# Kernel tuning notes

Hardware: AMD Instinct MI355X
Metric: run time of the kernel (lower is better)

The kernel has to match this reference:

```python
import jax, jax.numpy as jnp
import numpy as np

B = 32768

def _lin(x, w, b):
    return x @ w.T + b

def setup_inputs() -> dict:
    key = jax.random.key(0)
    ks = iter(jax.random.split(key, 40))
    def rn(shape, s=0.05):
        return jax.random.normal(next(ks), shape, dtype=jnp.float32) * s
    inp = {
        'img_feat': jax.random.normal(next(ks), (B, 256), dtype=jnp.float32),
        'instruction_idx': jax.random.randint(next(ks), (B, 1), 0, 4),
        '_hx': jax.random.normal(next(ks), (B, 256), dtype=jnp.float32),
        '_cx': jax.random.normal(next(ks), (B, 256), dtype=jnp.float32),
        'query': jax.random.normal(next(ks), (B, 256), dtype=jnp.float32),
        # parameters
        'emb': rn((4, 25), 1.0),
        'w_ta': rn((256, 25)), 'b_ta': rn((256,)),
        'w_ih': rn((1024, 512)), 'w_hh': rn((1024, 256)),
        'b_ih': rn((1024,)), 'b_hh': rn((1024,)),
        'w_q': rn((256, 256)), 'b_q': rn((256,)),
        'w_k': rn((256, 256)), 'b_k': rn((256,)),
        'w_ba': rn((512, 512)), 'b_ba': rn((512,)),
        'w_at': rn((256, 512)), 'b_at': rn((256,)),
        'w_p1': rn((128, 256)), 'b_p1': rn((128,)),
        'w_p2': rn((64, 128)), 'b_p2': rn((64,)),
        'w_p': rn((3, 64)), 'b_p': rn((3,)),
        'w_v1': rn((64, 256)), 'b_v1': rn((64,)),
        'w_v2': rn((32, 64)), 'b_v2': rn((32,)),
        'w_v': rn((1, 32)), 'b_v': rn((1,)),
    }
    return inp

def reference(img_feat, instruction_idx, _hx, _cx, query,
              emb, w_ta, b_ta, w_ih, w_hh, b_ih, b_hh,
              w_q, b_q, w_k, b_k, w_ba, b_ba, w_at, b_at,
              w_p1, b_p1, w_p2, b_p2, w_p, b_p,
              w_v1, b_v1, w_v2, b_v2, w_v, b_v):
    # embedding lookup [B,1,25] -> [B,25]
    we = emb[instruction_idx].reshape(instruction_idx.shape[0], -1)
    gated_att = jax.nn.sigmoid(_lin(we, w_ta, b_ta))          # [B,256]
    gated_fusion = img_feat * gated_att                        # [B,256]
    lstm_input = jnp.concatenate([gated_fusion, gated_att], 1) # [B,512]
    # LSTMCell (PyTorch gate order: i, f, g, o)
    gates = lstm_input @ w_ih.T + b_ih + _hx @ w_hh.T + b_hh   # [B,1024]
    i, f, g, o = jnp.split(gates, 4, axis=1)
    cx = jax.nn.sigmoid(f) * _cx + jax.nn.sigmoid(i) * jnp.tanh(g)
    hx = jax.nn.sigmoid(o) * jnp.tanh(cx)
    mlp_input = jnp.concatenate([gated_fusion, hx], 1)         # [B,512]
    mlp_attn = jax.nn.relu(_lin(mlp_input, w_ba, b_ba))        # [B,512]
    key_, val = jnp.split(mlp_attn, 2, axis=1)                 # [B,256] each
    w_q_out = jax.nn.relu(_lin(query, w_q, b_q))
    w_k_out = jax.nn.relu(_lin(key_, w_k, b_k))
    u_t = jnp.tanh(w_q_out + w_k_out)
    attention_vector = u_t * val
    attn_weight = jnp.concatenate([attention_vector, hx], 1)   # [B,512]
    attn_weight = jax.nn.relu(_lin(attn_weight, w_at, b_at))   # [B,256]
    pol = jax.nn.relu(_lin(attn_weight, w_p1, b_p1))
    pol = jax.nn.relu(_lin(pol, w_p2, b_p2))
    valh = jax.nn.relu(_lin(attn_weight, w_v1, b_v1))
    valh = jax.nn.relu(_lin(valh, w_v2, b_v2))
    return (_lin(valh, w_v, b_v), _lin(pol, w_p, b_p), hx, cx)
```

## Files before the change

kernel.cpp:

```cpp
#include <hip/hip_runtime.h>

typedef unsigned short u16;
typedef __bf16 bf16x8 __attribute__((ext_vector_type(8)));
typedef float f32x4 __attribute__((ext_vector_type(4)));
typedef u16 u16x8 __attribute__((ext_vector_type(8)));
typedef u16 u16x4 __attribute__((ext_vector_type(4)));

#define TM 64
#define LDP 264
#define BTOT 32768

#define OFF_WIH 0
#define OFF_WHH 524288
#define OFF_WQ  786432
#define OFF_WK  851968
#define OFF_WBA 917504
#define OFF_WAT 1179648
#define OFF_WP1 1310720
#define OFF_WP2 1343488
#define OFF_WV1 1351680
#define OFF_WV2 1368064

__device__ __forceinline__ float b2f(u16 h) {
    union { unsigned int u; float f; } v; v.u = ((unsigned int)h) << 16; return v.f;
}
__device__ __forceinline__ u16 f2b(float f) {
    union { float f; unsigned int u; } v; v.f = f;
    unsigned int u = v.u + 0x7fffu + ((v.u >> 16) & 1u);
    return (u16)(u >> 16);
}
__device__ __forceinline__ float sigm(float x) { return 1.0f / (1.0f + __expf(-x)); }
__device__ __forceinline__ float tanhfast(float x) { return 1.0f - 2.0f / (__expf(2.0f * x) + 1.0f); }
__device__ __forceinline__ float relu(float x) { return x > 0.0f ? x : 0.0f; }
__device__ __forceinline__ bf16x8 ld8(const u16* p) { return *(const bf16x8*)p; }
__device__ __forceinline__ f32x4 mfma16(bf16x8 a, bf16x8 b, f32x4 c) {
    return __builtin_amdgcn_mfma_f32_16x16x32_bf16(a, b, c, 0, 0, 0);
}

__device__ __forceinline__ bool detect_f32(const void* imgp) {
    const unsigned int* w = (const unsigned int*)imgp;
    int hits = 0;
    #pragma unroll
    for (int i = 0; i < 16; ++i) {
        int e0 = (w[i] >> 7) & 0xFF;
        hits += (e0 >= 100 && e0 <= 140) ? 1 : 0;
    }
    return hits < 10;
}

__device__ __forceinline__ float ldin(const void* p, size_t i, bool f32) {
    return f32 ? ((const float*)p)[i] : b2f(((const u16*)p)[i]);
}
__device__ __forceinline__ void stout_nt(void* o, size_t i, float v, bool f32) {
    if (f32) __builtin_nontemporal_store(v, (float*)o + i);
    else ((u16*)o)[i] = f2b(v);
}
__device__ __forceinline__ f32x4 ld4(const void* p, size_t i, bool f32) {
    if (f32) return __builtin_nontemporal_load((const f32x4*)((const float*)p + i));
    u16x4 q = *(const u16x4*)((const u16*)p + i);
    f32x4 r;
    #pragma unroll
    for (int j = 0; j < 4; ++j) r[j] = b2f(q[j]);
    return r;
}
__device__ __forceinline__ void st4(void* o, size_t i, f32x4 v, bool f32) {
    if (f32) __builtin_nontemporal_store(v, (f32x4*)((float*)o + i));
    else {
        u16x4 p;
        #pragma unroll
        for (int j = 0; j < 4; ++j) p[j] = f2b(v[j]);
        *(u16x4*)((u16*)o + i) = p;
    }
}
__device__ __forceinline__ bf16x8 ldg8f_nt(const void* p, size_t i, bool f32) {
    u16 t[8];
    if (f32) {
        const f32x4* q = (const f32x4*)((const float*)p + i);
        f32x4 a = __builtin_nontemporal_load(q);
        f32x4 b = __builtin_nontemporal_load(q + 1);
        #pragma unroll
        for (int j = 0; j < 4; ++j) { t[j] = f2b(a[j]); t[4 + j] = f2b(b[j]); }
    } else {
        *(u16x8*)t = *(const u16x8*)((const u16*)p + i);
    }
    return *(bf16x8*)t;
}

struct CvtArgs {
    const void* src[10];
    unsigned int nchunk[10];
    unsigned int off8[10];
    unsigned int Kdim[10];
    const void* det;
};

__global__ __launch_bounds__(256) void cvt_weights(CvtArgs a, u16* ws) {
    const bool f32 = detect_f32(a.det);
    const int p = blockIdx.x;
    const void* s = a.src[p];
    const unsigned int K = a.Kdim[p];
    const unsigned int KK = K >> 5;
    const unsigned int msk = KK - 1u;
    const unsigned int sh = 31 - __clz((int)KK);
    const unsigned int n = a.nchunk[p];
    for (unsigned int g = blockIdx.y * blockDim.x + threadIdx.x; g < n;
         g += gridDim.y * blockDim.x) {
        const unsigned int lane = g & 63u;
        const unsigned int fi = g >> 6;
        const unsigned int kk = fi & msk;
        const unsigned int tn = fi >> sh;
        const unsigned int row = tn * 16u + (lane & 15u);
        const unsigned int col = kk * 32u + ((lane >> 4) << 3);
        const size_t si = (size_t)row * K + col;
        u16 t[8];
        if (f32) {
            const f32x4* q = (const f32x4*)((const float*)s + si);
            f32x4 va = __builtin_nontemporal_load(q);
            f32x4 vb = __builtin_nontemporal_load(q + 1);
            #pragma unroll
            for (int j = 0; j < 4; ++j) { t[j] = f2b(va[j]); t[4 + j] = f2b(vb[j]); }
        } else {
            *(u16x8*)t = *(const u16x8*)((const u16*)s + si);
        }
        ((u16x8*)ws)[a.off8[p] + g] = *(u16x8*)t;
    }
}

__global__ __launch_bounds__(1024, 2) void ac_fused(
    const void* __restrict__ img, const int* __restrict__ insn,
    const void* __restrict__ hx_in, const void* __restrict__ cx_in,
    const void* __restrict__ query,
    const void* __restrict__ emb, const void* __restrict__ w_ta, const void* __restrict__ b_ta,
    const void* __restrict__ b_ih, const void* __restrict__ b_hh,
    const void* __restrict__ b_q, const void* __restrict__ b_k,
    const void* __restrict__ b_ba, const void* __restrict__ b_at,
    const void* __restrict__ b_p1, const void* __restrict__ b_p2,
    const void* __restrict__ w_p3, const void* __restrict__ b_p3,
    const void* __restrict__ b_v1, const void* __restrict__ b_v2,
    const void* __restrict__ w_v3, const void* __restrict__ b_v3,
    const u16* __restrict__ wsb, void* __restrict__ out)
{
    __shared__ __align__(16) u16 sGF[TM * LDP];
    __shared__ __align__(16) u16 sHX0[TM * LDP];
    __shared__ __align__(16) u16 sHX1[TM * LDP];
    __shared__ __align__(16) u16 sKEY[TM * LDP];
    __shared__ __align__(16) u16 sG[4 * LDP];
    __shared__ int sIDX[TM];

    const bool isf32 = detect_f32(img);
    const int tid  = threadIdx.x;
    const int lane = tid & 63;
    const int wv   = tid >> 6;
    const int l15  = lane & 15;
    const int quad = lane >> 4;
    const int q8   = quad * 8;
    const int q4   = quad * 4;
    const int ln8  = lane * 8;
    const int row0 = blockIdx.x * TM;

    if (tid < TM) sIDX[tid] = insn[row0 + tid];
    {
        int e = tid >> 8, n = tid & 255;
        float acc = ldin(b_ta, n, isf32);
        #pragma unroll
        for (int k = 0; k < 25; ++k)
            acc += ldin(emb, e * 25 + k, isf32) * ldin(w_ta, n * 25 + k, isf32);
        sG[e * LDP + n] = f2b(sigm(acc));
    }
    __syncthreads();

    for (int it = tid; it < TM * 32; it += 1024) {
        int r = it >> 5, c0 = (it & 31) << 3;
        int e = sIDX[r];
        u16x8 gv = *(const u16x8*)(sG + e * LDP + c0);
        float iv[8], hv[8];
        const size_t base = (size_t)(row0 + r) * 256 + c0;
        if (isf32) {
            const f32x4* ip = (const f32x4*)((const float*)img + base);
            const f32x4* hp = (const f32x4*)((const float*)hx_in + base);
            f32x4 a0 = __builtin_nontemporal_load(ip);
            f32x4 a1 = __builtin_nontemporal_load(ip + 1);
            f32x4 b0 = __builtin_nontemporal_load(hp);
            f32x4 b1 = __builtin_nontemporal_load(hp + 1);
            #pragma unroll
            for (int j = 0; j < 4; ++j) {
                iv[j] = a0[j]; iv[4 + j] = a1[j];
                hv[j] = b0[j]; hv[4 + j] = b1[j];
            }
        } else {
            u16x8 i8 = *(const u16x8*)((const u16*)img + base);
            u16x8 h8 = *(const u16x8*)((const u16*)hx_in + base);
            #pragma unroll
            for (int j = 0; j < 8; ++j) { iv[j] = b2f(i8[j]); hv[j] = b2f(h8[j]); }
        }
        u16x8 ov, hvv;
        #pragma unroll
        for (int j = 0; j < 8; ++j) {
            ov[j] = f2b(iv[j] * b2f(gv[j]));
            hvv[j] = f2b(hv[j]);
        }
        *(u16x8*)(sGF + r * LDP + c0) = ov;
        *(u16x8*)(sHX0 + r * LDP + c0) = hvv;
    }
    __syncthreads();

    {
        int eIdx[4];
        #pragma unroll
        for (int m = 0; m < 4; ++m) eIdx[m] = sIDX[m * 16 + l15];
        const u16* bih0 = wsb + OFF_WIH + ln8;
        const u16* bhh0 = wsb + OFF_WHH + ln8;
        const int c = wv;
        f32x4 acc[4][4] = {};
        #pragma unroll
        for (int kk = 0; kk < 8; ++kk) {
            bf16x8 a[4], b[4];
            #pragma unroll
            for (int m = 0; m < 4; ++m) a[m] = ld8(sGF + (m * 16 + l15) * LDP + kk * 32 + q8);
            #pragma unroll
            for (int g = 0; g < 4; ++g) b[g] = ld8(bih0 + (size_t)((g * 16 + c) * 16 + kk) * 512);
            #pragma unroll
            for (int g = 0; g < 4; ++g)
                #pragma unroll
                for (int m = 0; m < 4; ++m) acc[g][m] = mfma16(b[g], a[m], acc[g][m]);
        }
        #pragma unroll
        for (int kk = 0; kk < 8; ++kk) {
            bf16x8 a[4], b[4];
            #pragma unroll
            for (int m = 0; m < 4; ++m) a[m] = ld8(sG + eIdx[m] * LDP + kk * 32 + q8);
            #pragma unroll
            for (int g = 0; g < 4; ++g) b[g] = ld8(bih0 + (size_t)((g * 16 + c) * 16 + 8 + kk) * 512);
            #pragma unroll
            for (int g = 0; g < 4; ++g)
                #pragma unroll
                for (int m = 0; m < 4; ++m) acc[g][m] = mfma16(b[g], a[m], acc[g][m]);
        }
        #pragma unroll
        for (int kk = 0; kk < 8; ++kk) {
            bf16x8 a[4], b[4];
            #pragma unroll
            for (int m = 0; m < 4; ++m) a[m] = ld8(sHX0 + (m * 16 + l15) * LDP + kk * 32 + q8);
            #pragma unroll
            for (int g = 0; g < 4; ++g) b[g] = ld8(bhh0 + (size_t)((g * 16 + c) * 8 + kk) * 512);
            #pragma unroll
            for (int g = 0; g < 4; ++g)
                #pragma unroll
                for (int m = 0; m < 4; ++m) acc[g][m] = mfma16(b[g], a[m], acc[g][m]);
        }
        const int nbase = c * 16 + q4;
        float bI[4], bF[4], bG[4], bO[4];
        #pragma unroll
        for (int r = 0; r < 4; ++r) {
            bI[r] = ldin(b_ih,       nbase + r, isf32) + ldin(b_hh,       nbase + r, isf32);
            bF[r] = ldin(b_ih, 256 + nbase + r, isf32) + ldin(b_hh, 256 + nbase + r, isf32);
            bG[r] = ldin(b_ih, 512 + nbase + r, isf32) + ldin(b_hh, 512 + nbase + r, isf32);
            bO[r] = ldin(b_ih, 768 + nbase + r, isf32) + ldin(b_hh, 768 + nbase + r, isf32);
        }
        #pragma unroll
        for (int m = 0; m < 4; ++m) {
            const int batch = m * 16 + l15;
            const size_t gbase = (size_t)(row0 + batch) * 256 + nbase;
            f32x4 cxo = ld4(cx_in, gbase, isf32);
            f32x4 hnv, cnv; u16x4 hpk;
            #pragma unroll
            for (int r = 0; r < 4; ++r) {
                const float iv = sigm(acc[0][m][r] + bI[r]);
                const float fv = sigm(acc[1][m][r] + bF[r]);
                const float gv = tanhfast(acc[2][m][r] + bG[r]);
                const float ov = sigm(acc[3][m][r] + bO[r]);
                const float cn = fv * cxo[r] + iv * gv;
                const float hn = ov * tanhfast(cn);
                cnv[r] = cn; hnv[r] = hn; hpk[r] = f2b(hn);
            }
            st4(out, (size_t)(4 * BTOT) + gbase, hnv, isf32);
            st4(out, (size_t)(4 * BTOT) + (size_t)256 * BTOT + gbase, cnv, isf32);
            *(u16x4*)(sHX1 + batch * LDP + nbase) = hpk;
        }
    }
    __syncthreads();

    {
        f32x4 acc[2][4] = {};
        const u16* bb0 = wsb + OFF_WBA + ln8;
        #pragma unroll
        for (int kk = 0; kk < 8; ++kk) {
            bf16x8 a[4], b[2];
            #pragma unroll
            for (int m = 0; m < 4; ++m) a[m] = ld8(sGF + (m * 16 + l15) * LDP + kk * 32 + q8);
            #pragma unroll
            for (int t = 0; t < 2; ++t) b[t] = ld8(bb0 + (size_t)((wv * 2 + t) * 16 + kk) * 512);
            #pragma unroll
            for (int t = 0; t < 2; ++t)
                #pragma unroll
                for (int m = 0; m < 4; ++m) acc[t][m] = mfma16(b[t], a[m], acc[t][m]);
        }
        #pragma unroll
        for (int kk = 0; kk < 8; ++kk) {
            bf16x8 a[4], b[2];
            #pragma unroll
            for (int m = 0; m < 4; ++m) a[m] = ld8(sHX1 + (m * 16 + l15) * LDP + kk * 32 + q8);
            #pragma unroll
            for (int t = 0; t < 2; ++t) b[t] = ld8(bb0 + (size_t)((wv * 2 + t) * 16 + 8 + kk) * 512);
            #pragma unroll
            for (int t = 0; t < 2; ++t)
                #pragma unroll
                for (int m = 0; m < 4; ++m) acc[t][m] = mfma16(b[t], a[m], acc[t][m]);
        }
        #pragma unroll
        for (int t = 0; t < 2; ++t) {
            const int colb = (wv * 2 + t) * 16 + q4;
            float bb[4];
            #pragma unroll
            for (int r = 0; r < 4; ++r) bb[r] = ldin(b_ba, colb + r, isf32);
            u16* dst = (colb < 256) ? (sKEY + colb) : (sHX0 + (colb - 256));
            #pragma unroll
            for (int m = 0; m < 4; ++m) {
                u16x4 pk;
                #pragma unroll
                for (int r = 0; r < 4; ++r) pk[r] = f2b(relu(acc[t][m][r] + bb[r]));
                *(u16x4*)(dst + (m * 16 + l15) * LDP) = pk;
            }
        }
    }
    __syncthreads();

    {
        f32x4 cq[4] = {}, ck[4] = {};
        const u16* bq0 = wsb + OFF_WQ + ln8;
        const u16* bk0 = wsb + OFF_WK + ln8;
        #pragma unroll
        for (int kk = 0; kk < 8; ++kk) {
            bf16x8 aq[4], ak[4], bqf, bkf;
            #pragma unroll
            for (int m = 0; m < 4; ++m) {
                aq[m] = ldg8f_nt(query, (size_t)(row0 + m * 16 + l15) * 256 + kk * 32 + q8, isf32);
                ak[m] = ld8(sKEY + (m * 16 + l15) * LDP + kk * 32 + q8);
            }
            bqf = ld8(bq0 + (size_t)(wv * 8 + kk) * 512);
            bkf = ld8(bk0 + (size_t)(wv * 8 + kk) * 512);
            #pragma unroll
            for (int m = 0; m < 4; ++m) {
                cq[m] = mfma16(bqf, aq[m], cq[m]);
                ck[m] = mfma16(bkf, ak[m], ck[m]);
            }
        }
        const int nbase = wv * 16 + q4;
        float bqv[4], bkv[4];
        #pragma unroll
        for (int r = 0; r < 4; ++r) {
            bqv[r] = ldin(b_q, nbase + r, isf32);
            bkv[r] = ldin(b_k, nbase + r, isf32);
        }
        #pragma unroll
        for (int m = 0; m < 4; ++m) {
            const int batch = m * 16 + l15;
            u16x4 vv = *(const u16x4*)(sHX0 + batch * LDP + nbase);
            u16x4 pk;
            #pragma unroll
            for (int r = 0; r < 4; ++r) {
                const float u = tanhfast(relu(cq[m][r] + bqv[r]) + relu(ck[m][r] + bkv[r]));
                pk[r] = f2b(u * b2f(vv[r]));
            }
            *(u16x4*)(sGF + batch * LDP + nbase) = pk;
        }
    }
    __syncthreads();

    {
        f32x4 acc[4] = {};
        const u16* bb0 = wsb + OFF_WAT + ln8;
        #pragma unroll
        for (int kk = 0; kk < 8; ++kk) {
            bf16x8 a[4], b;
            #pragma unroll
            for (int m = 0; m < 4; ++m) a[m] = ld8(sGF + (m * 16 + l15) * LDP + kk * 32 + q8);
            b = ld8(bb0 + (size_t)(wv * 16 + kk) * 512);
            #pragma unroll
            for (int m = 0; m < 4; ++m) acc[m] = mfma16(b, a[m], acc[m]);
        }
        #pragma unroll
        for (int kk = 0; kk < 8; ++kk) {
            bf16x8 a[4], b;
            #pragma unroll
            for (int m = 0; m < 4; ++m) a[m] = ld8(sHX1 + (m * 16 + l15) * LDP + kk * 32 + q8);
            b = ld8(bb0 + (size_t)(wv * 16 + 8 + kk) * 512);
            #pragma unroll
            for (int m = 0; m < 4; ++m) acc[m] = mfma16(b, a[m], acc[m]);
        }
        const int nbase = wv * 16 + q4;
        float bb[4];
        #pragma unroll
        for (int r = 0; r < 4; ++r) bb[r] = ldin(b_at, nbase + r, isf32);
        #pragma unroll
        for (int m = 0; m < 4; ++m) {
            u16x4 pk;
            #pragma unroll
            for (int r = 0; r < 4; ++r) pk[r] = f2b(relu(acc[m][r] + bb[r]));
            *(u16x4*)(sKEY + (m * 16 + l15) * LDP + nbase) = pk;
        }
    }
    __syncthreads();

    {
        const int m = wv & 3, half = wv >> 2;
        const int batch = m * 16 + l15;
        bf16x8 afr[8];
        #pragma unroll
        for (int kk = 0; kk < 8; ++kk) afr[kk] = ld8(sKEY + batch * LDP + kk * 32 + q8);
        {
            f32x4 acc[2] = {};
            #pragma unroll
            for (int kk = 0; kk < 8; ++kk)
                #pragma unroll
                for (int t = 0; t < 2; ++t)
                    acc[t] = mfma16(ld8(wsb + OFF_WP1 + (size_t)((half * 2 + t) * 8 + kk) * 512 + ln8), afr[kk], acc[t]);
            #pragma unroll
            for (int t = 0; t < 2; ++t) {
                const int colb = (half * 2 + t) * 16 + q4;
                u16x4 pk;
                #pragma unroll
                for (int r = 0; r < 4; ++r) pk[r] = f2b(relu(acc[t][r] + ldin(b_p1, colb + r, isf32)));
                *(u16x4*)(sHX0 + batch * LDP + colb) = pk;
            }
        }
        {
            f32x4 acc = {};
            #pragma unroll
            for (int kk = 0; kk < 8; ++kk)
                acc = mfma16(ld8(wsb + OFF_WV1 + (size_t)(half * 8 + kk) * 512 + ln8), afr[kk], acc);
            const int colb = half * 16 + q4;
            u16x4 pk;
            #pragma unroll
            for (int r = 0; r < 4; ++r) pk[r] = f2b(relu(acc[r] + ldin(b_v1, colb + r, isf32)));
            *(u16x4*)(sHX0 + batch * LDP + 128 + colb) = pk;
        }
    }
    __syncthreads();

    {
        const int m = wv & 3, half = wv >> 2;
        const int batch = m * 16 + l15;
        const u16* a0 = sHX0 + batch * LDP;
        bf16x8 ap[4], av2[2];
        #pragma unroll
        for (int kk = 0; kk < 4; ++kk) ap[kk] = ld8(a0 + kk * 32 + q8);
        #pragma unroll
        for (int kk = 0; kk < 2; ++kk) av2[kk] = ld8(a0 + 128 + kk * 32 + q8);
        {
            f32x4 acc = {};
            #pragma unroll
            for (int kk = 0; kk < 4; ++kk)
                acc = mfma16(ld8(wsb + OFF_WP2 + (size_t)(half * 4 + kk) * 512 + ln8), ap[kk], acc);
            const int colb = half * 16 + q4;
            u16x4 pk;
            #pragma unroll
            for (int r = 0; r < 4; ++r) pk[r] = f2b(relu(acc[r] + ldin(b_p2, colb + r, isf32)));
            *(u16x4*)(sGF + batch * LDP + colb) = pk;
        }
        if (half < 2) {
            f32x4 acc = {};
            #pragma unroll
            for (int kk = 0; kk < 2; ++kk)
                acc = mfma16(ld8(wsb + OFF_WV2 + (size_t)(half * 2 + kk) * 512 + ln8), av2[kk], acc);
            const int colb = half * 16 + q4;
            u16x4 pk;
            #pragma unroll
            for (int r = 0; r < 4; ++r) pk[r] = f2b(relu(acc[r] + ldin(b_v2, colb + r, isf32)));
            *(u16x4*)(sGF + batch * LDP + 64 + colb) = pk;
        }
    }
    __syncthreads();

    if (tid < TM * 4) {
        const int r = tid >> 2, o = tid & 3;
        const int grow = row0 + r;
        const u16* rowp = sGF + r * LDP;
        if (o < 3) {
            float acc = ldin(b_p3, o, isf32);
            #pragma unroll
            for (int k = 0; k < 64; ++k) acc += b2f(rowp[k]) * ldin(w_p3, o * 64 + k, isf32);
            stout_nt(out, (size_t)BTOT + (size_t)grow * 3 + o, acc, isf32);
        } else {
            float acc = ldin(b_v3, 0, isf32);
            #pragma unroll
            for (int k = 0; k < 32; ++k) acc += b2f(rowp[64 + k]) * ldin(w_v3, k, isf32);
            stout_nt(out, (size_t)grow, acc, isf32);
        }
    }
}

extern "C" void kernel_launch(void* const* d_in, const int* in_sizes, int n_in,
                              void* d_out, int out_size, void* d_ws, size_t ws_size,
                              hipStream_t stream) {
    u16* ws = (u16*)d_ws;

    CvtArgs ca;
    const int srcIdx[10] = {8, 9, 12, 14, 16, 18, 20, 22, 26, 28};
    const unsigned int ns[10]   = {524288, 262144, 65536, 65536, 262144, 131072, 32768, 8192, 16384, 2048};
    const unsigned int off[10]  = {OFF_WIH, OFF_WHH, OFF_WQ, OFF_WK, OFF_WBA, OFF_WAT, OFF_WP1, OFF_WP2, OFF_WV1, OFF_WV2};
    const unsigned int kd[10]   = {512, 256, 256, 256, 512, 512, 256, 128, 256, 64};
    for (int i = 0; i < 10; ++i) {
        ca.src[i] = d_in[srcIdx[i]];
        ca.nchunk[i] = ns[i] / 8;
        ca.off8[i] = off[i] / 8;
        ca.Kdim[i] = kd[i];
    }
    ca.det = d_in[0];
    cvt_weights<<<dim3(10, 64), dim3(256), 0, stream>>>(ca, ws);

    ac_fused<<<dim3(BTOT / TM), dim3(1024), 0, stream>>>(
        d_in[0], (const int*)d_in[1], d_in[2], d_in[3], d_in[4],
        d_in[5], d_in[6], d_in[7],
        d_in[10], d_in[11],
        d_in[13], d_in[15],
        d_in[17], d_in[19],
        d_in[21], d_in[23],
        d_in[24], d_in[25],
        d_in[27], d_in[29],
        d_in[30], d_in[31],
        (const u16*)d_ws, d_out);
}
```

Measured before the change: 421.9 us.

## Double-buffer operand loads in fused GEMM stages and overlap query prefetch with barrier

Each MFMA stage now uses explicit ping-pong register buffers, so the next k-step's LDS and weight loads are issued before the current step's MFMAs. The separate k-sections of each GEMM are merged into one software-pipelined loop. The first query/weight fragments for the Q/K stage are prefetched before the barrier. The weight conversion kernel now iterates over source-contiguous elements for coalesced reads and scatters into the tiled layout. Extra live registers may raise pressure at the kernel's 1024-thread, 2-block launch bounds and risk spills.

```diff
diff --git a/kernel.cpp b/kernel.cpp
--- a/kernel.cpp
+++ b/kernel.cpp
@@ -99,19 +99,17 @@
     const int p = blockIdx.x;
     const void* s = a.src[p];
     const unsigned int K = a.Kdim[p];
-    const unsigned int KK = K >> 5;
-    const unsigned int msk = KK - 1u;
-    const unsigned int sh = 31 - __clz((int)KK);
+    const unsigned int sh = 31 - __clz((int)(K >> 5));
+    const unsigned int cpr = K >> 3;
+    const unsigned int csh = sh + 2;
     const unsigned int n = a.nchunk[p];
-    for (unsigned int g = blockIdx.y * blockDim.x + threadIdx.x; g < n;
-         g += gridDim.y * blockDim.x) {
-        const unsigned int lane = g & 63u;
-        const unsigned int fi = g >> 6;
-        const unsigned int kk = fi & msk;
-        const unsigned int tn = fi >> sh;
-        const unsigned int row = tn * 16u + (lane & 15u);
-        const unsigned int col = kk * 32u + ((lane >> 4) << 3);
-        const size_t si = (size_t)row * K + col;
+    for (unsigned int e = blockIdx.y * blockDim.x + threadIdx.x; e < n;
+         e += gridDim.y * blockDim.x) {
+        const unsigned int row  = e >> csh;
+        const unsigned int colc = e & (cpr - 1u);
+        const unsigned int g = ((((row >> 4) << sh) + (colc >> 2)) << 6)
+                             + ((colc & 3u) << 4) + (row & 15u);
+        const size_t si = ((size_t)row << (csh + 3)) + (colc << 3);
         u16 t[8];
         if (f32) {
             const f32x4* q = (const f32x4*)((const float*)s + si);
@@ -211,43 +209,48 @@
         const u16* bih0 = wsb + OFF_WIH + ln8;
         const u16* bhh0 = wsb + OFF_WHH + ln8;
         const int c = wv;
+
+        auto t1LA = [&](int s, bf16x8 (&a)[4]) {
+            const int sec = s >> 3, kq = (s & 7) * 32 + q8;
+            #pragma unroll
+            for (int m = 0; m < 4; ++m) {
+                const u16* src = (sec == 0) ? (sGF + (m * 16 + l15) * LDP + kq)
+                               : (sec == 1) ? (sG + eIdx[m] * LDP + kq)
+                                            : (sHX0 + (m * 16 + l15) * LDP + kq);
+                a[m] = ld8(src);
+            }
+        };
+        auto t1LB = [&](int s, bf16x8 (&b)[4]) {
+            const int sec = s >> 3, kk = s & 7;
+            #pragma unroll
+            for (int g = 0; g < 4; ++g)
+                b[g] = (sec < 2)
+                     ? ld8(bih0 + (size_t)((g * 16 + c) * 16 + sec * 8 + kk) * 512)
+                     : ld8(bhh0 + (size_t)((g * 16 + c) * 8 + kk) * 512);
+        };
+
         f32x4 acc[4][4] = {};
-        #pragma unroll
-        for (int kk = 0; kk < 8; ++kk) {
-            bf16x8 a[4], b[4];
-            #pragma unroll
-            for (int m = 0; m < 4; ++m) a[m] = ld8(sGF + (m * 16 + l15) * LDP + kk * 32 + q8);
-            #pragma unroll
-            for (int g = 0; g < 4; ++g) b[g] = ld8(bih0 + (size_t)((g * 16 + c) * 16 + kk) * 512);
-            #pragma unroll
-            for (int g = 0; g < 4; ++g)
-                #pragma unroll
-                for (int m = 0; m < 4; ++m) acc[g][m] = mfma16(b[g], a[m], acc[g][m]);
-        }
-        #pragma unroll
-        for (int kk = 0; kk < 8; ++kk) {
-            bf16x8 a[4], b[4];
-            #pragma unroll
-            for (int m = 0; m < 4; ++m) a[m] = ld8(sG + eIdx[m] * LDP + kk * 32 + q8);
-            #pragma unroll
-            for (int g = 0; g < 4; ++g) b[g] = ld8(bih0 + (size_t)((g * 16 + c) * 16 + 8 + kk) * 512);
-            #pragma unroll
-            for (int g = 0; g < 4; ++g)
-                #pragma unroll
-                for (int m = 0; m < 4; ++m) acc[g][m] = mfma16(b[g], a[m], acc[g][m]);
-        }
-        #pragma unroll
-        for (int kk = 0; kk < 8; ++kk) {
-            bf16x8 a[4], b[4];
-            #pragma unroll
-            for (int m = 0; m < 4; ++m) a[m] = ld8(sHX0 + (m * 16 + l15) * LDP + kk * 32 + q8);
-            #pragma unroll
-            for (int g = 0; g < 4; ++g) b[g] = ld8(bhh0 + (size_t)((g * 16 + c) * 8 + kk) * 512);
-            #pragma unroll
-            for (int g = 0; g < 4; ++g)
-                #pragma unroll
-                for (int m = 0; m < 4; ++m) acc[g][m] = mfma16(b[g], a[m], acc[g][m]);
-        }
+        bf16x8 aP[4], bP[4], aN[4], bN[4];
+        t1LA(0, aP); t1LB(0, bP);
+        #pragma unroll
+        for (int s = 0; s < 24; ++s) {
+            if (s + 1 < 24) {
+                if (s & 1) { t1LA(s + 1, aP); t1LB(s + 1, bP); }
+                else       { t1LA(s + 1, aN); t1LB(s + 1, bN); }
+            }
+            if (s & 1) {
+                #pragma unroll
+                for (int g = 0; g < 4; ++g)
+                    #pragma unroll
+                    for (int m = 0; m < 4; ++m) acc[g][m] = mfma16(bN[g], aN[m], acc[g][m]);
+            } else {
+                #pragma unroll
+                for (int g = 0; g < 4; ++g)
+                    #pragma unroll
+                    for (int m = 0; m < 4; ++m) acc[g][m] = mfma16(bP[g], aP[m], acc[g][m]);
+            }
+        }
+
         const int nbase = c * 16 + q4;
         float bI[4], bF[4], bG[4], bO[4];
         #pragma unroll
@@ -281,31 +284,42 @@
     __syncthreads();
 
     {
+        const u16* bb0 = wsb + OFF_WBA + ln8;
+        auto t2LA = [&](int s, bf16x8 (&a)[4]) {
+            const int sec = s >> 3, kq = (s & 7) * 32 + q8;
+            const u16* base = (sec == 0) ? sGF : sHX1;
+            #pragma unroll
+            for (int m = 0; m < 4; ++m) a[m] = ld8(base + (m * 16 + l15) * LDP + kq);
+        };
+        auto t2LB = [&](int s, bf16x8 (&b)[2]) {
+            const int sec = s >> 3, kk = s & 7;
+            #pragma unroll
+            for (int t = 0; t < 2; ++t)
+                b[t] = ld8(bb0 + (size_t)((wv * 2 + t) * 16 + sec * 8 + kk) * 512);
+        };
+
         f32x4 acc[2][4] = {};
-        const u16* bb0 = wsb + OFF_WBA + ln8;
-        #pragma unroll
-        for (int kk = 0; kk < 8; ++kk) {
-            bf16x8 a[4], b[2];
-            #pragma unroll
-            for (int m = 0; m < 4; ++m) a[m] = ld8(sGF + (m * 16 + l15) * LDP + kk * 32 + q8);
-            #pragma unroll
-            for (int t = 0; t < 2; ++t) b[t] = ld8(bb0 + (size_t)((wv * 2 + t) * 16 + kk) * 512);
-            #pragma unroll
-            for (int t = 0; t < 2; ++t)
-                #pragma unroll
-                for (int m = 0; m < 4; ++m) acc[t][m] = mfma16(b[t], a[m], acc[t][m]);
-        }
-        #pragma unroll
-        for (int kk = 0; kk < 8; ++kk) {
-            bf16x8 a[4], b[2];
-            #pragma unroll
-            for (int m = 0; m < 4; ++m) a[m] = ld8(sHX1 + (m * 16 + l15) * LDP + kk * 32 + q8);
-            #pragma unroll
-            for (int t = 0; t < 2; ++t) b[t] = ld8(bb0 + (size_t)((wv * 2 + t) * 16 + 8 + kk) * 512);
-            #pragma unroll
-            for (int t = 0; t < 2; ++t)
-                #pragma unroll
-                for (int m = 0; m < 4; ++m) acc[t][m] = mfma16(b[t], a[m], acc[t][m]);
+        {
+            bf16x8 aP[4], aN[4], bP[2], bN[2];
+            t2LA(0, aP); t2LB(0, bP);
+            #pragma unroll
+            for (int s = 0; s < 16; ++s) {
+                if (s + 1 < 16) {
+                    if (s & 1) { t2LA(s + 1, aP); t2LB(s + 1, bP); }
+                    else       { t2LA(s + 1, aN); t2LB(s + 1, bN); }
+                }
+                if (s & 1) {
+                    #pragma unroll
+                    for (int t = 0; t < 2; ++t)
+                        #pragma unroll
+                        for (int m = 0; m < 4; ++m) acc[t][m] = mfma16(bN[t], aN[m], acc[t][m]);
+                } else {
+                    #pragma unroll
+                    for (int t = 0; t < 2; ++t)
+                        #pragma unroll
+                        for (int m = 0; m < 4; ++m) acc[t][m] = mfma16(bP[t], aP[m], acc[t][m]);
+                }
+            }
         }
         #pragma unroll
         for (int t = 0; t < 2; ++t) {
@@ -322,27 +336,57 @@
                 *(u16x4*)(dst + (m * 16 + l15) * LDP) = pk;
             }
         }
-    }
-    __syncthreads();
-
-    {
-        f32x4 cq[4] = {}, ck[4] = {};
+
         const u16* bq0 = wsb + OFF_WQ + ln8;
         const u16* bk0 = wsb + OFF_WK + ln8;
-        #pragma unroll
-        for (int kk = 0; kk < 8; ++kk) {
-            bf16x8 aq[4], ak[4], bqf, bkf;
-            #pragma unroll
-            for (int m = 0; m < 4; ++m) {
-                aq[m] = ldg8f_nt(query, (size_t)(row0 + m * 16 + l15) * 256 + kk * 32 + q8, isf32);
-                ak[m] = ld8(sKEY + (m * 16 + l15) * LDP + kk * 32 + q8);
-            }
-            bqf = ld8(bq0 + (size_t)(wv * 8 + kk) * 512);
-            bkf = ld8(bk0 + (size_t)(wv * 8 + kk) * 512);
-            #pragma unroll
-            for (int m = 0; m < 4; ++m) {
-                cq[m] = mfma16(bqf, aq[m], cq[m]);
-                ck[m] = mfma16(bkf, ak[m], ck[m]);
+        bf16x8 aqP[4], aqN[4];
+        bf16x8 bqP, bkP, bqN, bkN;
+        #pragma unroll
+        for (int m = 0; m < 4; ++m)
+            aqP[m] = ldg8f_nt(query, (size_t)(row0 + m * 16 + l15) * 256 + q8, isf32);
+        bqP = ld8(bq0 + (size_t)(wv * 8) * 512);
+        bkP = ld8(bk0 + (size_t)(wv * 8) * 512);
+
+        __syncthreads();
+
+        f32x4 cq[4] = {}, ck[4] = {};
+        bf16x8 akP[4], akN[4];
+        #pragma unroll
+        for (int m = 0; m < 4; ++m) akP[m] = ld8(sKEY + (m * 16 + l15) * LDP + q8);
+        #pragma unroll
+        for (int s = 0; s < 8; ++s) {
+            if (s + 1 < 8) {
+                const int kq = (s + 1) * 32 + q8;
+                if (s & 1) {
+                    #pragma unroll
+                    for (int m = 0; m < 4; ++m) {
+                        aqP[m] = ldg8f_nt(query, (size_t)(row0 + m * 16 + l15) * 256 + kq, isf32);
+                        akP[m] = ld8(sKEY + (m * 16 + l15) * LDP + kq);
+                    }
+                    bqP = ld8(bq0 + (size_t)(wv * 8 + s + 1) * 512);
+                    bkP = ld8(bk0 + (size_t)(wv * 8 + s + 1) * 512);
+                } else {
+                    #pragma unroll
+                    for (int m = 0; m < 4; ++m) {
+                        aqN[m] = ldg8f_nt(query, (size_t)(row0 + m * 16 + l15) * 256 + kq, isf32);
+                        akN[m] = ld8(sKEY + (m * 16 + l15) * LDP + kq);
+                    }
+                    bqN = ld8(bq0 + (size_t)(wv * 8 + s + 1) * 512);
+                    bkN = ld8(bk0 + (size_t)(wv * 8 + s + 1) * 512);
+                }
+            }
+            if (s & 1) {
+                #pragma unroll
+                for (int m = 0; m < 4; ++m) {
+                    cq[m] = mfma16(bqN, aqN[m], cq[m]);
+                    ck[m] = mfma16(bkN, akN[m], ck[m]);
+                }
+            } else {
+                #pragma unroll
+                for (int m = 0; m < 4; ++m) {
+                    cq[m] = mfma16(bqP, aqP[m], cq[m]);
+                    ck[m] = mfma16(bkP, akP[m], ck[m]);
+                }
             }
         }
         const int nbase = wv * 16 + q4;
@@ -368,25 +412,36 @@
     __syncthreads();
 
     {
+        const u16* bb0 = wsb + OFF_WAT + ln8;
+        auto t4LA = [&](int s, bf16x8 (&a)[4]) {
+            const int sec = s >> 3, kq = (s & 7) * 32 + q8;
+            const u16* base = (sec == 0) ? sGF : sHX1;
+            #pragma unroll
+            for (int m = 0; m < 4; ++m) a[m] = ld8(base + (m * 16 + l15) * LDP + kq);
+        };
         f32x4 acc[4] = {};
-        const u16* bb0 = wsb + OFF_WAT + ln8;
-        #pragma unroll
-        for (int kk = 0; kk < 8; ++kk) {
-            bf16x8 a[4], b;
-            #pragma unroll
-            for (int m = 0; m < 4; ++m) a[m] = ld8(sGF + (m * 16 + l15) * LDP + kk * 32 + q8);
-            b = ld8(bb0 + (size_t)(wv * 16 + kk) * 512);
-            #pragma unroll
-            for (int m = 0; m < 4; ++m) acc[m] = mfma16(b, a[m], acc[m]);
-        }
-        #pragma unroll
-        for (int kk = 0; kk < 8; ++kk) {
-            bf16x8 a[4], b;
-            #pragma unroll
-            for (int m = 0; m < 4; ++m) a[m] = ld8(sHX1 + (m * 16 + l15) * LDP + kk * 32 + q8);
-            b = ld8(bb0 + (size_t)(wv * 16 + 8 + kk) * 512);
-            #pragma unroll
-            for (int m = 0; m < 4; ++m) acc[m] = mfma16(b, a[m], acc[m]);
+        bf16x8 aP[4], aN[4], bP, bN;
+        t4LA(0, aP);
+        bP = ld8(bb0 + (size_t)(wv * 16) * 512);
+        #pragma unroll
+        for (int s = 0; s < 16; ++s) {
+            if (s + 1 < 16) {
+                const int sec = (s + 1) >> 3, kk = (s + 1) & 7;
+                if (s & 1) {
+                    t4LA(s + 1, aP);
+                    bP = ld8(bb0 + (size_t)(wv * 16 + sec * 8 + kk) * 512);
+                } else {
+                    t4LA(s + 1, aN);
+                    bN = ld8(bb0 + (size_t)(wv * 16 + sec * 8 + kk) * 512);
+                }
+            }
+            if (s & 1) {
+                #pragma unroll
+                for (int m = 0; m < 4; ++m) acc[m] = mfma16(bN, aN[m], acc[m]);
+            } else {
+                #pragma unroll
+                for (int m = 0; m < 4; ++m) acc[m] = mfma16(bP, aP[m], acc[m]);
+            }
         }
         const int nbase = wv * 16 + q4;
         float bb[4];
```

New measurement: 452.5 us. 7.2% more time.

## Prefetch next-stage weights and inputs before barriers and defer LSTM output stores

Applied to the files above, without the earlier changes.

Before each __syncthreads, every stage now issues the first global loads of the next stage's weight and activation fragments (W_ba, W_q/W_k plus the query tile, W_at, W_p1/W_v1, W_p2/W_v2), so their latency overlaps the barrier wait. The cx load is moved ahead of the LSTM gate GEMM, and the hx/cx global stores are held in registers and written after the barrier, overlapping with the next GEMM. The tiny final-head weights are staged once into shared memory instead of being re-read from global in the inner loop. In exchange, register pressure rises, which may cut occupancy or cause spills.

```diff
diff --git a/kernel.cpp b/kernel.cpp
--- a/kernel.cpp
+++ b/kernel.cpp
@@ -145,6 +145,7 @@
     __shared__ __align__(16) u16 sHX1[TM * LDP];
     __shared__ __align__(16) u16 sKEY[TM * LDP];
     __shared__ __align__(16) u16 sG[4 * LDP];
+    __shared__ float sW3[224];
     __shared__ int sIDX[TM];
 
     const bool isf32 = detect_f32(img);
@@ -204,6 +205,7 @@
     }
     __syncthreads();
 
+    f32x4 hnS[4], cnS[4];
     {
         int eIdx[4];
         #pragma unroll
@@ -211,6 +213,12 @@
         const u16* bih0 = wsb + OFF_WIH + ln8;
         const u16* bhh0 = wsb + OFF_WHH + ln8;
         const int c = wv;
+        const int nbase = c * 16 + q4;
+        f32x4 cxo[4];
+        #pragma unroll
+        for (int m = 0; m < 4; ++m)
+            cxo[m] = ld4(cx_in, (size_t)(row0 + m * 16 + l15) * 256 + nbase, isf32);
+
         f32x4 acc[4][4] = {};
         #pragma unroll
         for (int kk = 0; kk < 8; ++kk) {
@@ -248,7 +256,6 @@
                 #pragma unroll
                 for (int m = 0; m < 4; ++m) acc[g][m] = mfma16(b[g], a[m], acc[g][m]);
         }
-        const int nbase = c * 16 + q4;
         float bI[4], bF[4], bG[4], bO[4];
         #pragma unroll
         for (int r = 0; r < 4; ++r) {
@@ -260,48 +267,63 @@
         #pragma unroll
         for (int m = 0; m < 4; ++m) {
             const int batch = m * 16 + l15;
-            const size_t gbase = (size_t)(row0 + batch) * 256 + nbase;
-            f32x4 cxo = ld4(cx_in, gbase, isf32);
-            f32x4 hnv, cnv; u16x4 hpk;
+            u16x4 hpk;
             #pragma unroll
             for (int r = 0; r < 4; ++r) {
                 const float iv = sigm(acc[0][m][r] + bI[r]);
                 const float fv = sigm(acc[1][m][r] + bF[r]);
                 const float gv = tanhfast(acc[2][m][r] + bG[r]);
                 const float ov = sigm(acc[3][m][r] + bO[r]);
-                const float cn = fv * cxo[r] + iv * gv;
+                const float cn = fv * cxo[m][r] + iv * gv;
                 const float hn = ov * tanhfast(cn);
-                cnv[r] = cn; hnv[r] = hn; hpk[r] = f2b(hn);
-            }
-            st4(out, (size_t)(4 * BTOT) + gbase, hnv, isf32);
-            st4(out, (size_t)(4 * BTOT) + (size_t)256 * BTOT + gbase, cnv, isf32);
+                cnS[m][r] = cn; hnS[m][r] = hn; hpk[r] = f2b(hn);
+            }
             *(u16x4*)(sHX1 + batch * LDP + nbase) = hpk;
         }
     }
-    __syncthreads();
-
-    {
+
+    const u16* bba0 = wsb + OFF_WBA + ln8;
+    bf16x8 h2a[4], h2b[2];
+    #pragma unroll
+    for (int m = 0; m < 4; ++m) h2a[m] = ld8(sGF + (m * 16 + l15) * LDP + q8);
+    #pragma unroll
+    for (int t = 0; t < 2; ++t) h2b[t] = ld8(bba0 + (size_t)((wv * 2 + t) * 16) * 512);
+    __syncthreads();
+
+    {
+        {
+            const int nbase = wv * 16 + q4;
+            #pragma unroll
+            for (int m = 0; m < 4; ++m) {
+                const size_t gbase = (size_t)(row0 + m * 16 + l15) * 256 + nbase;
+                st4(out, (size_t)(4 * BTOT) + gbase, hnS[m], isf32);
+                st4(out, (size_t)(4 * BTOT) + (size_t)256 * BTOT + gbase, cnS[m], isf32);
+            }
+        }
         f32x4 acc[2][4] = {};
-        const u16* bb0 = wsb + OFF_WBA + ln8;
+        #pragma unroll
+        for (int t = 0; t < 2; ++t)
+            #pragma unroll
+            for (int m = 0; m < 4; ++m) acc[t][m] = mfma16(h2b[t], h2a[m], acc[t][m]);
+        #pragma unroll
+        for (int kk = 1; kk < 8; ++kk) {
+            bf16x8 a[4], b[2];
+            #pragma unroll
+            for (int m = 0; m < 4; ++m) a[m] = ld8(sGF + (m * 16 + l15) * LDP + kk * 32 + q8);
+            #pragma unroll
+            for (int t = 0; t < 2; ++t) b[t] = ld8(bba0 + (size_t)((wv * 2 + t) * 16 + kk) * 512);
+            #pragma unroll
+            for (int t = 0; t < 2; ++t)
+                #pragma unroll
+                for (int m = 0; m < 4; ++m) acc[t][m] = mfma16(b[t], a[m], acc[t][m]);
+        }
         #pragma unroll
         for (int kk = 0; kk < 8; ++kk) {
             bf16x8 a[4], b[2];
             #pragma unroll
-            for (int m = 0; m < 4; ++m) a[m] = ld8(sGF + (m * 16 + l15) * LDP + kk * 32 + q8);
-            #pragma unroll
-            for (int t = 0; t < 2; ++t) b[t] = ld8(bb0 + (size_t)((wv * 2 + t) * 16 + kk) * 512);
-            #pragma unroll
-            for (int t = 0; t < 2; ++t)
-                #pragma unroll
-                for (int m = 0; m < 4; ++m) acc[t][m] = mfma16(b[t], a[m], acc[t][m]);
-        }
-        #pragma unroll
-        for (int kk = 0; kk < 8; ++kk) {
-            bf16x8 a[4], b[2];
-            #pragma unroll
             for (int m = 0; m < 4; ++m) a[m] = ld8(sHX1 + (m * 16 + l15) * LDP + kk * 32 + q8);
             #pragma unroll
-            for (int t = 0; t < 2; ++t) b[t] = ld8(bb0 + (size_t)((wv * 2 + t) * 16 + 8 + kk) * 512);
+            for (int t = 0; t < 2; ++t) b[t] = ld8(bba0 + (size_t)((wv * 2 + t) * 16 + 8 + kk) * 512);
             #pragma unroll
             for (int t = 0; t < 2; ++t)
                 #pragma unroll
@@ -323,14 +345,31 @@
             }
         }
     }
+
+    const u16* bq0 = wsb + OFF_WQ + ln8;
+    const u16* bk0 = wsb + OFF_WK + ln8;
+    bf16x8 h3aq[4], h3bq, h3bk;
+    #pragma unroll
+    for (int m = 0; m < 4; ++m)
+        h3aq[m] = ldg8f_nt(query, (size_t)(row0 + m * 16 + l15) * 256 + q8, isf32);
+    h3bq = ld8(bq0 + (size_t)(wv * 8) * 512);
+    h3bk = ld8(bk0 + (size_t)(wv * 8) * 512);
     __syncthreads();
 
     {
         f32x4 cq[4] = {}, ck[4] = {};
-        const u16* bq0 = wsb + OFF_WQ + ln8;
-        const u16* bk0 = wsb + OFF_WK + ln8;
-        #pragma unroll
-        for (int kk = 0; kk < 8; ++kk) {
+        {
+            bf16x8 ak0[4];
+            #pragma unroll
+            for (int m = 0; m < 4; ++m) ak0[m] = ld8(sKEY + (m * 16 + l15) * LDP + q8);
+            #pragma unroll
+            for (int m = 0; m < 4; ++m) {
+                cq[m] = mfma16(h3bq, h3aq[m], cq[m]);
+                ck[m] = mfma16(h3bk, ak0[m], ck[m]);
+            }
+        }
+        #pragma unroll
+        for (int kk = 1; kk < 8; ++kk) {
             bf16x8 aq[4], ak[4], bqf, bkf;
             #pragma unroll
             for (int m = 0; m < 4; ++m) {
@@ -365,26 +404,38 @@
             *(u16x4*)(sGF + batch * LDP + nbase) = pk;
         }
     }
+
+    const u16* bat0 = wsb + OFF_WAT + ln8;
+    bf16x8 h4b0 = ld8(bat0 + (size_t)(wv * 16) * 512);
+    bf16x8 h4b1 = ld8(bat0 + (size_t)(wv * 16 + 1) * 512);
     __syncthreads();
 
     {
         f32x4 acc[4] = {};
-        const u16* bb0 = wsb + OFF_WAT + ln8;
+        #pragma unroll
+        for (int kk = 0; kk < 2; ++kk) {
+            bf16x8 a[4];
+            #pragma unroll
+            for (int m = 0; m < 4; ++m) a[m] = ld8(sGF + (m * 16 + l15) * LDP + kk * 32 + q8);
+            const bf16x8 b = (kk == 0) ? h4b0 : h4b1;
+            #pragma unroll
+            for (int m = 0; m < 4; ++m) acc[m] = mfma16(b, a[m], acc[m]);
+        }
+        #pragma unroll
+        for (int kk = 2; kk < 8; ++kk) {
+            bf16x8 a[4], b;
+            #pragma unroll
+            for (int m = 0; m < 4; ++m) a[m] = ld8(sGF + (m * 16 + l15) * LDP + kk * 32 + q8);
+            b = ld8(bat0 + (size_t)(wv * 16 + kk) * 512);
+            #pragma unroll
+            for (int m = 0; m < 4; ++m) acc[m] = mfma16(b, a[m], acc[m]);
+        }
         #pragma unroll
         for (int kk = 0; kk < 8; ++kk) {
             bf16x8 a[4], b;
             #pragma unroll
-            for (int m = 0; m < 4; ++m) a[m] = ld8(sGF + (m * 16 + l15) * LDP + kk * 32 + q8);
-            b = ld8(bb0 + (size_t)(wv * 16 + kk) * 512);
-            #pragma unroll
-            for (int m = 0; m < 4; ++m) acc[m] = mfma16(b, a[m], acc[m]);
-        }
-        #pragma unroll
-        for (int kk = 0; kk < 8; ++kk) {
-            bf16x8 a[4], b;
-            #pragma unroll
             for (int m = 0; m < 4; ++m) a[m] = ld8(sHX1 + (m * 16 + l15) * LDP + kk * 32 + q8);
-            b = ld8(bb0 + (size_t)(wv * 16 + 8 + kk) * 512);
+            b = ld8(bat0 + (size_t)(wv * 16 + 8 + kk) * 512);
             #pragma unroll
             for (int m = 0; m < 4; ++m) acc[m] = mfma16(b, a[m], acc[m]);
         }
@@ -400,24 +451,34 @@
             *(u16x4*)(sKEY + (m * 16 + l15) * LDP + nbase) = pk;
         }
     }
-    __syncthreads();
-
-    {
-        const int m = wv & 3, half = wv >> 2;
-        const int batch = m * 16 + l15;
+
+    const int t56m = wv & 3, t56h = wv >> 2;
+    bf16x8 h5p0 = ld8(wsb + OFF_WP1 + (size_t)((t56h * 2 + 0) * 8) * 512 + ln8);
+    bf16x8 h5p1 = ld8(wsb + OFF_WP1 + (size_t)((t56h * 2 + 1) * 8) * 512 + ln8);
+    bf16x8 h5v0 = ld8(wsb + OFF_WV1 + (size_t)(t56h * 8) * 512 + ln8);
+    __syncthreads();
+
+    bf16x8 h6p[4], h6v[2];
+    {
+        if (tid < 224)
+            sW3[tid] = (tid < 192) ? ldin(w_p3, tid, isf32)
+                                   : ldin(w_v3, tid - 192, isf32);
+        const int batch = t56m * 16 + l15;
         bf16x8 afr[8];
         #pragma unroll
         for (int kk = 0; kk < 8; ++kk) afr[kk] = ld8(sKEY + batch * LDP + kk * 32 + q8);
         {
             f32x4 acc[2] = {};
-            #pragma unroll
-            for (int kk = 0; kk < 8; ++kk)
+            acc[0] = mfma16(h5p0, afr[0], acc[0]);
+            acc[1] = mfma16(h5p1, afr[0], acc[1]);
+            #pragma unroll
+            for (int kk = 1; kk < 8; ++kk)
                 #pragma unroll
                 for (int t = 0; t < 2; ++t)
-                    acc[t] = mfma16(ld8(wsb + OFF_WP1 + (size_t)((half * 2 + t) * 8 + kk) * 512 + ln8), afr[kk], acc[t]);
+                    acc[t] = mfma16(ld8(wsb + OFF_WP1 + (size_t)((t56h * 2 + t) * 8 + kk) * 512 + ln8), afr[kk], acc[t]);
             #pragma unroll
             for (int t = 0; t < 2; ++t) {
-                const int colb = (half * 2 + t) * 16 + q4;
+                const int colb = (t56h * 2 + t) * 16 + q4;
                 u16x4 pk;
                 #pragma unroll
                 for (int r = 0; r < 4; ++r) pk[r] = f2b(relu(acc[t][r] + ldin(b_p1, colb + r, isf32)));
@@ -426,21 +487,27 @@
         }
         {
             f32x4 acc = {};
-            #pragma unroll
-            for (int kk = 0; kk < 8; ++kk)
-                acc = mfma16(ld8(wsb + OFF_WV1 + (size_t)(half * 8 + kk) * 512 + ln8), afr[kk], acc);
-            const int colb = half * 16 + q4;
+            acc = mfma16(h5v0, afr[0], acc);
+            #pragma unroll
+            for (int kk = 1; kk < 8; ++kk)
+                acc = mfma16(ld8(wsb + OFF_WV1 + (size_t)(t56h * 8 + kk) * 512 + ln8), afr[kk], acc);
+            const int colb = t56h * 16 + q4;
             u16x4 pk;
             #pragma unroll
             for (int r = 0; r < 4; ++r) pk[r] = f2b(relu(acc[r] + ldin(b_v1, colb + r, isf32)));
             *(u16x4*)(sHX0 + batch * LDP + 128 + colb) = pk;
         }
-    }
-    __syncthreads();
-
-    {
-        const int m = wv & 3, half = wv >> 2;
-        const int batch = m * 16 + l15;
+        #pragma unroll
+        for (int kk = 0; kk < 4; ++kk)
+            h6p[kk] = ld8(wsb + OFF_WP2 + (size_t)(t56h * 4 + kk) * 512 + ln8);
+        #pragma unroll
+        for (int kk = 0; kk < 2; ++kk)
+            h6v[kk] = ld8(wsb + OFF_WV2 + (size_t)(t56h * 2 + kk) * 512 + ln8);
+    }
+    __syncthreads();
+
+    {
+        const int batch = t56m * 16 + l15;
         const u16* a0 = sHX0 + batch * LDP;
         bf16x8 ap[4], av2[2];
         #pragma unroll
@@ -450,20 +517,18 @@
         {
             f32x4 acc = {};
             #pragma unroll
-            for (int kk = 0; kk < 4; ++kk)
-                acc = mfma16(ld8(wsb + OFF_WP2 + (size_t)(half * 4 + kk) * 512 + ln8), ap[kk], acc);
-            const int colb = half * 16 + q4;
+            for (int kk = 0; kk < 4; ++kk) acc = mfma16(h6p[kk], ap[kk], acc);
+            const int colb = t56h * 16 + q4;
             u16x4 pk;
             #pragma unroll
             for (int r = 0; r < 4; ++r) pk[r] = f2b(relu(acc[r] + ldin(b_p2, colb + r, isf32)));
             *(u16x4*)(sGF + batch * LDP + colb) = pk;
         }
-        if (half < 2) {
+        if (t56h < 2) {
             f32x4 acc = {};
             #pragma unroll
-            for (int kk = 0; kk < 2; ++kk)
-                acc = mfma16(ld8(wsb + OFF_WV2 + (size_t)(half * 2 + kk) * 512 + ln8), av2[kk], acc);
-            const int colb = half * 16 + q4;
+            for (int kk = 0; kk < 2; ++kk) acc = mfma16(h6v[kk], av2[kk], acc);
+            const int colb = t56h * 16 + q4;
             u16x4 pk;
             #pragma unroll
             for (int r = 0; r < 4; ++r) pk[r] = f2b(relu(acc[r] + ldin(b_v2, colb + r, isf32)));
@@ -479,12 +544,12 @@
         if (o < 3) {
             float acc = ldin(b_p3, o, isf32);
             #pragma unroll
-            for (int k = 0; k < 64; ++k) acc += b2f(rowp[k]) * ldin(w_p3, o * 64 + k, isf32);
+            for (int k = 0; k < 64; ++k) acc += b2f(rowp[k]) * sW3[o * 64 + k];
             stout_nt(out, (size_t)BTOT + (size_t)grow * 3 + o, acc, isf32);
         } else {
             float acc = ldin(b_v3, 0, isf32);
             #pragma unroll
-            for (int k = 0; k < 32; ++k) acc += b2f(rowp[64 + k]) * ldin(w_v3, k, isf32);
+            for (int k = 0; k < 32; ++k) acc += b2f(rowp[64 + k]) * sW3[192 + k];
             stout_nt(out, (size_t)grow, acc, isf32);
         }
     }
```

Result: slower. 439.8 us (+4.2%).

## Precompute gate table in prep kernel, coalesce weight conversion, prefetch inputs early

Applied to the files above, without the earlier changes.

The 4x256 sigmoid gate table, which every block of the fused kernel used to recompute, is now built once by an extra block in the weight-conversion kernel and stored in the workspace, so fused blocks only copy it. The weight conversion loop now walks the source row-major for coalesced reads and scatters writes into the MFMA tile layout. The fused kernel also issues its img/hx loads before the first barrier, so their latency overlaps the index and table setup. In exchange the loads are held in more registers across the barrier, and the writes in the conversion kernel are scattered.

```diff
diff --git a/kernel.cpp b/kernel.cpp
--- a/kernel.cpp
+++ b/kernel.cpp
@@ -20,6 +20,7 @@
 #define OFF_WP2 1343488
 #define OFF_WV1 1351680
 #define OFF_WV2 1368064
+#define OFF_G   1370112
 
 __device__ __forceinline__ float b2f(u16 h) {
     union { unsigned int u; float f; } v; v.u = ((unsigned int)h) << 16; return v.f;
@@ -91,32 +92,46 @@
     unsigned int nchunk[10];
     unsigned int off8[10];
     unsigned int Kdim[10];
+    const void* emb;
+    const void* w_ta;
+    const void* b_ta;
     const void* det;
 };
 
 __global__ __launch_bounds__(256) void cvt_weights(CvtArgs a, u16* ws) {
     const bool f32 = detect_f32(a.det);
     const int p = blockIdx.x;
+    if (p == 10) {
+        if (blockIdx.y == 0) {
+            for (int j = threadIdx.x; j < 1024; j += 256) {
+                int e = j >> 8, n = j & 255;
+                float acc = ldin(a.b_ta, n, f32);
+                #pragma unroll
+                for (int k = 0; k < 25; ++k)
+                    acc += ldin(a.emb, e * 25 + k, f32) * ldin(a.w_ta, n * 25 + k, f32);
+                ws[OFF_G + j] = f2b(sigm(acc));
+            }
+        }
+        return;
+    }
     const void* s = a.src[p];
     const unsigned int K = a.Kdim[p];
-    const unsigned int KK = K >> 5;
-    const unsigned int msk = KK - 1u;
-    const unsigned int sh = 31 - __clz((int)KK);
+    const unsigned int sh = 31 - __clz((int)(K >> 5));
+    const unsigned int cpr = K >> 3;
+    const unsigned int csh = sh + 2;
     const unsigned int n = a.nchunk[p];
-    for (unsigned int g = blockIdx.y * blockDim.x + threadIdx.x; g < n;
-         g += gridDim.y * blockDim.x) {
-        const unsigned int lane = g & 63u;
-        const unsigned int fi = g >> 6;
-        const unsigned int kk = fi & msk;
-        const unsigned int tn = fi >> sh;
-        const unsigned int row = tn * 16u + (lane & 15u);
-        const unsigned int col = kk * 32u + ((lane >> 4) << 3);
-        const size_t si = (size_t)row * K + col;
+    for (unsigned int e = blockIdx.y * blockDim.x + threadIdx.x; e < n;
+         e += gridDim.y * blockDim.x) {
+        const unsigned int row  = e >> csh;
+        const unsigned int colc = e & (cpr - 1u);
+        const unsigned int g = ((((row >> 4) << sh) + (colc >> 2)) << 6)
+                             + ((colc & 3u) << 4) + (row & 15u);
+        const size_t si = ((size_t)e) << 3;
         u16 t[8];
         if (f32) {
             const f32x4* q = (const f32x4*)((const float*)s + si);
-            f32x4 va = __builtin_nontemporal_load(q);
-            f32x4 vb = __builtin_nontemporal_load(q + 1);
+            f32x4 va = *q;
+            f32x4 vb = *(q + 1);
             #pragma unroll
             for (int j = 0; j < 4; ++j) { t[j] = f2b(va[j]); t[4 + j] = f2b(vb[j]); }
         } else {
@@ -130,7 +145,6 @@
     const void* __restrict__ img, const int* __restrict__ insn,
     const void* __restrict__ hx_in, const void* __restrict__ cx_in,
     const void* __restrict__ query,
-    const void* __restrict__ emb, const void* __restrict__ w_ta, const void* __restrict__ b_ta,
     const void* __restrict__ b_ih, const void* __restrict__ b_hh,
     const void* __restrict__ b_q, const void* __restrict__ b_k,
     const void* __restrict__ b_ba, const void* __restrict__ b_at,
@@ -158,49 +172,62 @@
     const int ln8  = lane * 8;
     const int row0 = blockIdx.x * TM;
 
+    const int r0s = tid >> 5, c0s = (tid & 31) << 3;
+    const int r1s = (tid + 1024) >> 5;
+    float iv0[8], hv0[8], iv1[8], hv1[8];
+    {
+        const size_t base0 = (size_t)(row0 + r0s) * 256 + c0s;
+        const size_t base1 = (size_t)(row0 + r1s) * 256 + c0s;
+        if (isf32) {
+            const f32x4* ip0 = (const f32x4*)((const float*)img + base0);
+            const f32x4* hp0 = (const f32x4*)((const float*)hx_in + base0);
+            const f32x4* ip1 = (const f32x4*)((const float*)img + base1);
+            const f32x4* hp1 = (const f32x4*)((const float*)hx_in + base1);
+            f32x4 a0 = __builtin_nontemporal_load(ip0);
+            f32x4 a1 = __builtin_nontemporal_load(ip0 + 1);
+            f32x4 b0 = __builtin_nontemporal_load(hp0);
+            f32x4 b1 = __builtin_nontemporal_load(hp0 + 1);
+            f32x4 c0 = __builtin_nontemporal_load(ip1);
+            f32x4 c1 = __builtin_nontemporal_load(ip1 + 1);
+            f32x4 d0 = __builtin_nontemporal_load(hp1);
+            f32x4 d1 = __builtin_nontemporal_load(hp1 + 1);
+            #pragma unroll
+            for (int j = 0; j < 4; ++j) {
+                iv0[j] = a0[j]; iv0[4 + j] = a1[j];
+                hv0[j] = b0[j]; hv0[4 + j] = b1[j];
+                iv1[j] = c0[j]; iv1[4 + j] = c1[j];
+                hv1[j] = d0[j]; hv1[4 + j] = d1[j];
+            }
+        } else {
+            u16x8 i80 = *(const u16x8*)((const u16*)img + base0);
+            u16x8 h80 = *(const u16x8*)((const u16*)hx_in + base0);
+            u16x8 i81 = *(const u16x8*)((const u16*)img + base1);
+            u16x8 h81 = *(const u16x8*)((const u16*)hx_in + base1);
+            #pragma unroll
+            for (int j = 0; j < 8; ++j) {
+                iv0[j] = b2f(i80[j]); hv0[j] = b2f(h80[j]);
+                iv1[j] = b2f(i81[j]); hv1[j] = b2f(h81[j]);
+            }
+        }
+    }
     if (tid < TM) sIDX[tid] = insn[row0 + tid];
-    {
-        int e = tid >> 8, n = tid & 255;
-        float acc = ldin(b_ta, n, isf32);
-        #pragma unroll
-        for (int k = 0; k < 25; ++k)
-            acc += ldin(emb, e * 25 + k, isf32) * ldin(w_ta, n * 25 + k, isf32);
-        sG[e * LDP + n] = f2b(sigm(acc));
-    }
-    __syncthreads();
-
-    for (int it = tid; it < TM * 32; it += 1024) {
-        int r = it >> 5, c0 = (it & 31) << 3;
-        int e = sIDX[r];
-        u16x8 gv = *(const u16x8*)(sG + e * LDP + c0);
-        float iv[8], hv[8];
-        const size_t base = (size_t)(row0 + r) * 256 + c0;
-        if (isf32) {
-            const f32x4* ip = (const f32x4*)((const float*)img + base);
-            const f32x4* hp = (const f32x4*)((const float*)hx_in + base);
-            f32x4 a0 = __builtin_nontemporal_load(ip);
-            f32x4 a1 = __builtin_nontemporal_load(ip + 1);
-            f32x4 b0 = __builtin_nontemporal_load(hp);
-            f32x4 b1 = __builtin_nontemporal_load(hp + 1);
-            #pragma unroll
-            for (int j = 0; j < 4; ++j) {
-                iv[j] = a0[j]; iv[4 + j] = a1[j];
-                hv[j] = b0[j]; hv[4 + j] = b1[j];
-            }
-        } else {
-            u16x8 i8 = *(const u16x8*)((const u16*)img + base);
-            u16x8 h8 = *(const u16x8*)((const u16*)hx_in + base);
-            #pragma unroll
-            for (int j = 0; j < 8; ++j) { iv[j] = b2f(i8[j]); hv[j] = b2f(h8[j]); }
-        }
-        u16x8 ov, hvv;
+    sG[(tid >> 8) * LDP + (tid & 255)] = wsb[OFF_G + tid];
+    __syncthreads();
+
+    {
+        int e0 = sIDX[r0s], e1 = sIDX[r1s];
+        u16x8 gv0 = *(const u16x8*)(sG + e0 * LDP + c0s);
+        u16x8 gv1 = *(const u16x8*)(sG + e1 * LDP + c0s);
+        u16x8 ov0, hvv0, ov1, hvv1;
         #pragma unroll
         for (int j = 0; j < 8; ++j) {
-            ov[j] = f2b(iv[j] * b2f(gv[j]));
-            hvv[j] = f2b(hv[j]);
-        }
-        *(u16x8*)(sGF + r * LDP + c0) = ov;
-        *(u16x8*)(sHX0 + r * LDP + c0) = hvv;
+            ov0[j] = f2b(iv0[j] * b2f(gv0[j]));  hvv0[j] = f2b(hv0[j]);
+            ov1[j] = f2b(iv1[j] * b2f(gv1[j]));  hvv1[j] = f2b(hv1[j]);
+        }
+        *(u16x8*)(sGF + r0s * LDP + c0s) = ov0;
+        *(u16x8*)(sHX0 + r0s * LDP + c0s) = hvv0;
+        *(u16x8*)(sGF + r1s * LDP + c0s) = ov1;
+        *(u16x8*)(sHX0 + r1s * LDP + c0s) = hvv1;
     }
     __syncthreads();
 
@@ -506,12 +533,14 @@
         ca.off8[i] = off[i] / 8;
         ca.Kdim[i] = kd[i];
     }
+    ca.emb = d_in[5];
+    ca.w_ta = d_in[6];
+    ca.b_ta = d_in[7];
     ca.det = d_in[0];
-    cvt_weights<<<dim3(10, 64), dim3(256), 0, stream>>>(ca, ws);
+    cvt_weights<<<dim3(11, 64), dim3(256), 0, stream>>>(ca, ws);
 
     ac_fused<<<dim3(BTOT / TM), dim3(1024), 0, stream>>>(
         d_in[0], (const int*)d_in[1], d_in[2], d_in[3], d_in[4],
-        d_in[5], d_in[6], d_in[7],
         d_in[10], d_in[11],
         d_in[13], d_in[15],
         d_in[17], d_in[19],
```

Measured after the change: 405.8 us. 1.04x faster.
